# Optimization experiments

Hardware: AMD Instinct MI355X
Metric: run time of the kernel (lower is better)

## Reference

```python
import jax, jax.numpy as jnp
import numpy as np

REG = 1.0
LAM1 = REG * 0.1
LAM2 = REG * 0.15
TAU = 0.01
RHO = 1.99
SIGMA = 1.0 / TAU / 72.0


def epsilon(I):
    # I: (c,h,w,2) -> G: (c,h,w,4); symmetrized gradient stencil
    I0, I1 = I[..., 0], I[..., 1]
    g0 = I0 - jnp.pad(I0[:, :-1, :], ((0, 0), (1, 0), (0, 0)))
    g1 = jnp.pad(I0[:, :, 1:] - I0[:, :, :-1], ((0, 0), (0, 0), (1, 0)))
    g2 = I1 - jnp.pad(I1[:, :, :-1], ((0, 0), (0, 0), (1, 0)))
    g3 = jnp.pad(I1[:, 1:, :] - I1[:, :-1, :], ((0, 0), (0, 1), (0, 0)))
    return jnp.stack([g0, g1, g2, g3], axis=-1)


def epsilonT(G):
    # G: (c,h,w,4) -> I: (c,h,w,2); adjoint of epsilon
    g0, g1, g2, g3 = G[..., 0], G[..., 1], G[..., 2], G[..., 3]
    i0 = g0 - jnp.pad(g0[:, 1:, :], ((0, 0), (0, 1), (0, 0)))
    A = g1[:, :, 1:]
    i0 = i0 + jnp.pad(A, ((0, 0), (0, 0), (1, 0))) - jnp.pad(A, ((0, 0), (0, 0), (0, 1)))
    i1 = g2 - jnp.pad(g2[:, :, 1:], ((0, 0), (0, 0), (0, 1)))
    B = g3[:, :-1, :]
    i1 = i1 + jnp.pad(B, ((0, 0), (1, 0), (0, 0))) - jnp.pad(B, ((0, 0), (0, 1), (0, 0)))
    return jnp.stack([i0, i1], axis=-1)


def nabla(I):
    # I: (c,h,w) -> G: (c,h,w,2); forward differences, zero at far boundary
    g0 = jnp.pad(I[:, 1:, :] - I[:, :-1, :], ((0, 0), (0, 1), (0, 0)))
    g1 = jnp.pad(I[:, :, 1:] - I[:, :, :-1], ((0, 0), (0, 0), (0, 1)))
    return jnp.stack([g0, g1], axis=-1)


def nablaT(G):
    # G: (c,h,w,2) -> I: (c,h,w); negative divergence (adjoint of nabla)
    A = G[:, :-1, :, 0]
    B = G[:, :, :-1, 1]
    return (jnp.pad(A, ((0, 0), (1, 0), (0, 0))) - jnp.pad(A, ((0, 0), (0, 1), (0, 0)))
            + jnp.pad(B, ((0, 0), (0, 0), (1, 0))) - jnp.pad(B, ((0, 0), (0, 0), (0, 1))))


def prox_tau_fx(x, y):
    return (x + TAU * y) / (1.0 + TAU)


def prox_tau_fr(r):
    left = jnp.sqrt(jnp.sum(r ** 2, axis=3)) / (TAU * LAM1)
    return r - r / jnp.maximum(left, 1.0)[..., None]


def prox_sigma_g_conj(u):
    return u / jnp.maximum(jnp.sqrt(jnp.sum(u ** 2, axis=3)) / LAM2, 1.0)[..., None]


def setup_inputs() -> dict:
    key = jax.random.key(0)
    y = jax.random.normal(key, (3, 512, 512), dtype=jnp.float32)
    return {"y": y, "n_it_max": 30}


def reference(y, n_it_max):
    c, h, w = y.shape
    x2 = y
    r2 = jnp.zeros((c, h, w, 2), dtype=y.dtype)
    u2 = jnp.zeros((c, h, w, 4), dtype=y.dtype)

    def step(carry, _):
        x2, r2, u2 = carry
        tmp = TAU * epsilonT(u2)
        x = prox_tau_fx(x2 - nablaT(tmp), y)
        r = prox_tau_fr(r2 + tmp)
        u = prox_sigma_g_conj(u2 + SIGMA * epsilon(nabla(2.0 * x - x2) - (2.0 * r - r2)))
        x2 = x2 + RHO * (x - x2)
        r2 = r2 + RHO * (r - r2)
        u2 = u2 + RHO * (u - u2)
        return (x2, r2, u2), None

    (x2, r2, u2), _ = jax.lax.scan(step, (x2, r2, u2), None, length=n_it_max)
    return (x2, r2, u2)
```

## Files before the change

### kernel.cpp

```cpp
#include <hip/hip_runtime.h>
#include <type_traits>


#define H 512
#define W 512
#define C 3
#define HW (H * W)
#define CHW (C * H * W)
#define NPAIR 15

#define TW 64
#define TH 16

#define TAU     0.01f
#define LAM2    0.15f
#define RHO     1.99f
#define SIGMA   1.3888888888888888f
#define TL1     0.001f
#define INV_1PT (1.0f / 1.01f)

#define AR 22
#define AC 78
#define BR 18
#define BC 72
#define UR 20
#define UC 75

typedef _Float16 f16;
typedef __attribute__((ext_vector_type(4))) _Float16 h4;
typedef __attribute__((ext_vector_type(8))) _Float16 h8;


template <int MODE>
__global__ __launch_bounds__(256)
void fused2(const float* __restrict__ y,
            const float* __restrict__ srcX,
            const f16*   __restrict__ srcH,
            float*       __restrict__ dstX,
            f16*         __restrict__ dstH,
            float*       __restrict__ outp)
{
    __shared__ float sbA[3][AR][AC];
    __shared__ float sbB[3][BR][BC];
    __shared__ f16   su[UR][UC][4];

    const int tid = threadIdx.x;
    const int c   = blockIdx.z;
    const int i0  = blockIdx.y * TH;
    const int j0  = blockIdx.x * TW;
    const int cb  = c * HW;

    const bool edge = (MODE == 0) ||
                      (blockIdx.x == 0) || (blockIdx.x == W / TW - 1) ||
                      (blockIdx.y == 0) || (blockIdx.y == H / TH - 1);

    const f16* rSrc = srcH;
    const f16* uSrc = srcH + 2 * CHW;
    f16* rDst = dstH;
    f16* uDst = dstH ? dstH + 2 * CHW : nullptr;

    auto prox1 = [&](auto SAFE_c, int gi, int gjb,
                     const float* yv, const float* x2c, const float* r0c, const float* r1c,
                     const float* t0c, const float* t1c, const float* t0n, const float* t1w,
                     float* xb, float* rb0, float* rb1,
                     float* xn, float* rn0, float* rn1) {
        constexpr bool SAFE = decltype(SAFE_c)::value;
        const bool imH = SAFE ? true : (gi < H - 1);
        #pragma unroll
        for (int e = 0; e < 4; ++e) {
            const int gj = gjb + e;
            const bool jmW = SAFE ? true : (gj < W - 1);
            const float nT  = t0n[e] - (imH ? t0c[e] : 0.f) + t1w[e] - (jmW ? t1c[e] : 0.f);
            const float xv  = (x2c[e] - nT + TAU * yv[e]) * INV_1PT;
            xb[e] = 2.f * xv - x2c[e];
            const float rp0 = r0c[e] + t0c[e];
            const float rp1 = r1c[e] + t1c[e];
            const float ss  = rp0 * rp0 + rp1 * rp1;
            const float f   = 1.f - fminf(TL1 * rsqrtf(ss), 1.f);
            const float rv0 = rp0 * f, rv1 = rp1 * f;
            rb0[e] = 2.f * rv0 - r0c[e];
            rb1[e] = 2.f * rv1 - r1c[e];
            xn[e]  = x2c[e] + RHO * (xv - x2c[e]);
            rn0[e] = r0c[e] + RHO * (rv0 - r0c[e]);
            rn1[e] = r1c[e] + RHO * (rv1 - r1c[e]);
        }
    };

    auto tGlob = [&](auto SAFE_c, int gi, int gjb, int p,
                     float* t0c, float* t1c, float* t0n, float* t1w) {
        constexpr bool SAFE = decltype(SAFE_c)::value;
        const bool rowC  = SAFE || ((unsigned)gi < H);
        const bool cMain = SAFE || ((unsigned)gjb < W);
        const bool okC   = rowC && cMain;
        const bool rowN = SAFE || ((unsigned)(gi - 1) < H);
        const bool rowS = SAFE || ((unsigned)(gi + 1) < H);
        const bool cm1  = SAFE || ((unsigned)(gjb - 1) < W);
        const bool c4   = SAFE || ((unsigned)(gjb + 4) < W);
        const int pN = p - W, pS = p + W;
        auto L4 = [&](int pp, bool ok) -> h4 { h4 z = {}; if (ok) z = *(const h4*)(uSrc + 4 * pp); return z; };
        auto L8 = [&](int pp, bool ok) -> h8 { h8 z = {}; if (ok) z = *(const h8*)(uSrc + 4 * pp); return z; };
        const h4 nA = L4(pN - 1, rowN && cm1);
        const h8 nB = L8(pN,     rowN && cMain);
        const h8 nC = L8(pN + 2, rowN && cMain);
        const h4 nD = L4(pN + 4, rowN && c4);
        const h4 cA = L4(p - 1,  rowC && cm1);
        const h8 cB = L8(p,      okC);
        const h8 cC = L8(p + 2,  okC);
        const h4 cD = L4(p + 4,  rowC && c4);
        const h8 sB = L8(pS,     rowS && cMain);
        const h8 sC = L8(pS + 2, rowS && cMain);

        const float u0c[4] = {(float)cB[0], (float)cB[4], (float)cC[0], (float)cC[4]};
        const float u1c[5] = {(float)cB[1], (float)cB[5], (float)cC[1], (float)cC[5], (float)cD[1]};
        const float u2r[6] = {(float)cA[2], (float)cB[2], (float)cB[6], (float)cC[2], (float)cC[6], (float)cD[2]};
        const float u3c[5] = {(float)cA[3], (float)cB[3], (float)cB[7], (float)cC[3], (float)cC[7]};
        const float u0n[4] = {(float)nB[0], (float)nB[4], (float)nC[0], (float)nC[4]};
        const float u1n[5] = {(float)nB[1], (float)nB[5], (float)nC[1], (float)nC[5], (float)nD[1]};
        const float u3n[5] = {(float)nA[3], (float)nB[3], (float)nB[7], (float)nC[3], (float)nC[7]};
        const float u0s[4] = {(float)sB[0], (float)sB[4], (float)sC[0], (float)sC[4]};

        if constexpr (SAFE) {
            #pragma unroll
            for (int e = 0; e < 4; ++e) {
                t0c[e] = TAU * (u0c[e] - u0s[e] + u1c[e] - u1c[e + 1]);
                t1c[e] = TAU * (u2r[e + 1] - u2r[e + 2] + u3n[e + 1] - u3c[e + 1]);
                t0n[e] = TAU * (u0n[e] - u0c[e] + u1n[e] - u1n[e + 1]);
                t1w[e] = TAU * (u2r[e] - u2r[e + 1] + u3n[e] - u3c[e]);
            }
        } else {
            const bool im0 = gi > 0, imHl = gi < H - 1;
            #pragma unroll
            for (int e = 0; e < 4; ++e) {
                const int gj = gjb + e;
                const bool jm0 = gj > 0;
                t0c[e] = TAU * (u0c[e] - u0s[e] + (jm0 ? u1c[e] : 0.f) - u1c[e + 1]);
                t1c[e] = TAU * (u2r[e + 1] - u2r[e + 2] + u3n[e + 1] - (imHl ? u3c[e + 1] : 0.f));
                t0n[e] = im0 ? TAU * (u0n[e] - u0c[e] + (jm0 ? u1n[e] : 0.f) - u1n[e + 1]) : 0.f;
                t1w[e] = jm0 ? TAU * (u2r[e] - u2r[e + 1] + u3n[e] - (imHl ? u3c[e] : 0.f)) : 0.f;
            }
        }
    };

    auto loadA = [&](int rr, int s,
                     float* xA, float* xS, float* xN,
                     float* r0C, float* r0N, float* r1C, float* r1S) {
        const int lr = rr + 3, lc = s + 8;
        float4 v;
        xA[0] = sbA[0][lr][lc - 1];
        v = *(const float4*)&sbA[0][lr][lc]; xA[1]=v.x; xA[2]=v.y; xA[3]=v.z; xA[4]=v.w;
        xA[5] = sbA[0][lr][lc + 4];
        xS[0] = sbA[0][lr + 1][lc - 1];
        v = *(const float4*)&sbA[0][lr + 1][lc]; xS[1]=v.x; xS[2]=v.y; xS[3]=v.z; xS[4]=v.w;
        xS[5] = sbA[0][lr + 1][lc + 4];
        v = *(const float4*)&sbA[0][lr - 1][lc]; xN[0]=v.x; xN[1]=v.y; xN[2]=v.z; xN[3]=v.w;
        r0C[0] = sbA[1][lr][lc - 1];
        v = *(const float4*)&sbA[1][lr][lc]; r0C[1]=v.x; r0C[2]=v.y; r0C[3]=v.z; r0C[4]=v.w;
        v = *(const float4*)&sbA[1][lr - 1][lc]; r0N[0]=v.x; r0N[1]=v.y; r0N[2]=v.z; r0N[3]=v.w;
        r1C[0] = sbA[2][lr][lc - 1];
        v = *(const float4*)&sbA[2][lr][lc]; r1C[1]=v.x; r1C[2]=v.y; r1C[3]=v.z; r1C[4]=v.w;
        v = *(const float4*)&sbA[2][lr + 1][lc]; r1S[0]=v.x; r1S[1]=v.y; r1S[2]=v.z; r1S[3]=v.w;
    };

    auto s2core = [&](auto SAFE_c, int gi, int gjb,
                      const float* xA, const float* xS, const float* xN,
                      const float* r0C, const float* r0N, const float* r1C, const float* r1S,
                      const float* cu0, const float* cu1, const float* cu2, const float* cu3,
                      float* un0, float* un1, float* un2, float* un3) {
        constexpr bool SAFE = decltype(SAFE_c)::value;
        const bool im0 = SAFE ? true : (gi > 0);
        const bool imH = SAFE ? true : (gi < H - 1);
        #pragma unroll
        for (int e = 0; e < 4; ++e) {
            const int gj = gjb + e;
            const bool jm0 = SAFE ? true : (gj > 0);
            const bool jmW = SAFE ? true : (gj < W - 1);
            const float xC = xA[e + 1], xE = xA[e + 2], xW_ = xA[e];
            const float I0c = (imH ? xS[e + 1] - xC : 0.f) - r0C[e + 1];
            const float I0n = im0 ? (xC - xN[e] - r0N[e]) : 0.f;
            const float I0w = jm0 ? ((imH ? xS[e] - xW_ : 0.f) - r0C[e]) : 0.f;
            const float I1c = (jmW ? xE - xC : 0.f) - r1C[e + 1];
            const float I1w = jm0 ? (xC - xW_ - r1C[e]) : 0.f;
            const float I1s = imH ? ((jmW ? xS[e + 2] - xS[e + 1] : 0.f) - r1S[e]) : 0.f;
            const float g0 = I0c - I0n;
            const float g1 = jm0 ? (I0c - I0w) : 0.f;
            const float g2 = I1c - I1w;
            const float g3 = imH ? (I1s - I1c) : 0.f;
            const float up0 = cu0[e] + SIGMA * g0;
            const float up1 = cu1[e] + SIGMA * g1;
            const float up2 = cu2[e] + SIGMA * g2;
            const float up3 = cu3[e] + SIGMA * g3;
            const float ss  = up0 * up0 + up1 * up1 + up2 * up2 + up3 * up3;
            const float inv = fminf(LAM2 * rsqrtf(ss), 1.f);
            un0[e] = cu0[e] + RHO * (up0 * inv - cu0[e]);
            un1[e] = cu1[e] + RHO * (up1 * inv - cu1[e]);
            un2[e] = cu2[e] + RHO * (up2 * inv - cu2[e]);
            un3[e] = cu3[e] + RHO * (up3 * inv - cu3[e]);
        }
    };

    auto phaseA = [&](auto SAFE_c) {
        constexpr bool SAFE = decltype(SAFE_c)::value;
        for (int idx = tid; idx < AR * 18; idx += 256) {
            const int rw = idx / 18, rr = rw - 3;
            const int s  = 4 * (idx - rw * 18) - 4;
            const int gi = i0 + rr, gjb = j0 + s;
            const int p  = cb + gi * W + gjb;
            const bool rowC  = SAFE || ((unsigned)gi < H);
            const bool cMain = SAFE || ((unsigned)gjb < W);
            const bool okC   = rowC && cMain;

            float yv[4], x2c[4], r0c[4], r1c[4];
            if (okC) { *(float4*)yv = *(const float4*)(y + p); }
            else     { yv[0] = yv[1] = yv[2] = yv[3] = 0.f; }

            float t0c[4], t1c[4], t0n[4], t1w[4];
            if (MODE == 0) {
                #pragma unroll
                for (int e = 0; e < 4; ++e) {
                    x2c[e] = yv[e]; r0c[e] = 0.f; r1c[e] = 0.f;
                    t0c[e] = t1c[e] = t0n[e] = t1w[e] = 0.f;
                }
            } else {
                if (okC) {
                    *(float4*)x2c = *(const float4*)(srcX + p);
                    const h8 rv = *(const h8*)(rSrc + 2 * p);
                    #pragma unroll
                    for (int e = 0; e < 4; ++e) {
                        r0c[e] = (float)rv[2 * e];
                        r1c[e] = (float)rv[2 * e + 1];
                    }
                } else {
                    #pragma unroll
                    for (int e = 0; e < 4; ++e) { x2c[e] = 0.f; r0c[e] = 0.f; r1c[e] = 0.f; }
                }
                tGlob(SAFE_c, gi, gjb, p, t0c, t1c, t0n, t1w);
            }

            float xb[4], rb0[4], rb1[4], xn[4], rn0[4], rn1[4];
            prox1(SAFE_c, gi, gjb, yv, x2c, r0c, r1c, t0c, t1c, t0n, t1w,
                  xb, rb0, rb1, xn, rn0, rn1);

            *(float4*)&sbA[0][rr + 3][s + 8] = *(float4*)xb;
            *(float4*)&sbA[1][rr + 3][s + 8] = *(float4*)rb0;
            *(float4*)&sbA[2][rr + 3][s + 8] = *(float4*)rb1;
            if (rr >= -1 && rr <= 16) {
                *(float4*)&sbB[0][rr + 1][s + 4] = *(float4*)xn;
                *(float4*)&sbB[1][rr + 1][s + 4] = *(float4*)rn0;
                *(float4*)&sbB[2][rr + 1][s + 4] = *(float4*)rn1;
            }
        }
    };

    auto phaseB = [&](auto SAFE_c) {
        constexpr bool SAFE = decltype(SAFE_c)::value;
        for (int idx = tid; idx < UR * 18; idx += 256) {
            const int rw = idx / 18, rr = rw - 2;
            const int s  = 4 * (idx - rw * 18) - 4;
            const int gi = i0 + rr, gjb = j0 + s;
            const int p  = cb + gi * W + gjb;

            float xA[6], xS[6], xN[4], r0C[5], r0N[4], r1C[5], r1S[4];
            loadA(rr, s, xA, xS, xN, r0C, r0N, r1C, r1S);

            float cu0[4], cu1[4], cu2[4], cu3[4];
            if (MODE == 0) {
                #pragma unroll
                for (int e = 0; e < 4; ++e) { cu0[e] = cu1[e] = cu2[e] = cu3[e] = 0.f; }
            } else {
                const bool okC = SAFE || (((unsigned)gi < H) && ((unsigned)gjb < W));
                if (okC) {
                    const h8 a = *(const h8*)(uSrc + 4 * p);
                    const h8 b = *(const h8*)(uSrc + 4 * p + 8);
                    cu0[0]=(float)a[0]; cu1[0]=(float)a[1]; cu2[0]=(float)a[2]; cu3[0]=(float)a[3];
                    cu0[1]=(float)a[4]; cu1[1]=(float)a[5]; cu2[1]=(float)a[6]; cu3[1]=(float)a[7];
                    cu0[2]=(float)b[0]; cu1[2]=(float)b[1]; cu2[2]=(float)b[2]; cu3[2]=(float)b[3];
                    cu0[3]=(float)b[4]; cu1[3]=(float)b[5]; cu2[3]=(float)b[6]; cu3[3]=(float)b[7];
                } else {
                    #pragma unroll
                    for (int e = 0; e < 4; ++e) { cu0[e] = cu1[e] = cu2[e] = cu3[e] = 0.f; }
                }
            }

            float un0[4], un1[4], un2[4], un3[4];
            s2core(SAFE_c, gi, gjb, xA, xS, xN, r0C, r0N, r1C, r1S,
                   cu0, cu1, cu2, cu3, un0, un1, un2, un3);

            const int ur = rr + 2, uc = s + 6;
            if constexpr (SAFE) {
                h8 w0, w1;
                #pragma unroll
                for (int e = 0; e < 2; ++e) {
                    w0[4*e+0]=(f16)un0[e]; w0[4*e+1]=(f16)un1[e];
                    w0[4*e+2]=(f16)un2[e]; w0[4*e+3]=(f16)un3[e];
                }
                #pragma unroll
                for (int e = 2; e < 4; ++e) {
                    w1[4*(e-2)+0]=(f16)un0[e]; w1[4*(e-2)+1]=(f16)un1[e];
                    w1[4*(e-2)+2]=(f16)un2[e]; w1[4*(e-2)+3]=(f16)un3[e];
                }
                *(h8*)&su[ur][uc][0]     = w0;
                *(h8*)&su[ur][uc + 2][0] = w1;
            } else {
                #pragma unroll
                for (int e = 0; e < 4; ++e) {
                    const int gj = gjb + e;
                    const bool ok = ((unsigned)gi < H) && ((unsigned)gj < W);
                    h4 hv = {};
                    if (ok) { hv[0]=(f16)un0[e]; hv[1]=(f16)un1[e]; hv[2]=(f16)un2[e]; hv[3]=(f16)un3[e]; }
                    *(h4*)&su[ur][uc + e][0] = hv;
                }
            }
        }
    };

    auto phaseC = [&](auto SAFE_c) {
        constexpr bool SAFE = decltype(SAFE_c)::value;
        for (int idx = tid; idx < BR * 18; idx += 256) {
            const int rw = idx / 18, rr = rw - 1;
            const int s  = 4 * (idx - rw * 18) - 4;
            const int gi = i0 + rr, gjb = j0 + s;
            const int p  = cb + gi * W + gjb;
            const bool okC = SAFE || (((unsigned)gi < H) && ((unsigned)gjb < W));

            float yv[4];
            if (okC) { *(float4*)yv = *(const float4*)(y + p); }
            else     { yv[0] = yv[1] = yv[2] = yv[3] = 0.f; }

            float x2c[4], r0c[4], r1c[4];
            *(float4*)x2c = *(const float4*)&sbB[0][rr + 1][s + 4];
            *(float4*)r0c = *(const float4*)&sbB[1][rr + 1][s + 4];
            *(float4*)r1c = *(const float4*)&sbB[2][rr + 1][s + 4];

            h4 pN_[6], pC_[6], pS_[4];
            #pragma unroll
            for (int k = 0; k < 6; ++k) {
                pN_[k] = *(const h4*)&su[rr + 1][s + 5 + k][0];
                pC_[k] = *(const h4*)&su[rr + 2][s + 5 + k][0];
            }
            #pragma unroll
            for (int k = 0; k < 4; ++k)
                pS_[k] = *(const h4*)&su[rr + 3][s + 6 + k][0];

            const float u0c[4] = {(float)pC_[1][0], (float)pC_[2][0], (float)pC_[3][0], (float)pC_[4][0]};
            const float u1c[5] = {(float)pC_[1][1], (float)pC_[2][1], (float)pC_[3][1], (float)pC_[4][1], (float)pC_[5][1]};
            const float u2r[6] = {(float)pC_[0][2], (float)pC_[1][2], (float)pC_[2][2], (float)pC_[3][2], (float)pC_[4][2], (float)pC_[5][2]};
            const float u3c[5] = {(float)pC_[0][3], (float)pC_[1][3], (float)pC_[2][3], (float)pC_[3][3], (float)pC_[4][3]};
            const float u0n[4] = {(float)pN_[1][0], (float)pN_[2][0], (float)pN_[3][0], (float)pN_[4][0]};
            const float u1n[5] = {(float)pN_[1][1], (float)pN_[2][1], (float)pN_[3][1], (float)pN_[4][1], (float)pN_[5][1]};
            const float u3n[5] = {(float)pN_[0][3], (float)pN_[1][3], (float)pN_[2][3], (float)pN_[3][3], (float)pN_[4][3]};
            const float u0s[4] = {(float)pS_[0][0], (float)pS_[1][0], (float)pS_[2][0], (float)pS_[3][0]};

            float t0c[4], t1c[4], t0n[4], t1w[4];
            if constexpr (SAFE) {
                #pragma unroll
                for (int e = 0; e < 4; ++e) {
                    t0c[e] = TAU * (u0c[e] - u0s[e] + u1c[e] - u1c[e + 1]);
                    t1c[e] = TAU * (u2r[e + 1] - u2r[e + 2] + u3n[e + 1] - u3c[e + 1]);
                    t0n[e] = TAU * (u0n[e] - u0c[e] + u1n[e] - u1n[e + 1]);
                    t1w[e] = TAU * (u2r[e] - u2r[e + 1] + u3n[e] - u3c[e]);
                }
            } else {
                const bool im0 = gi > 0, imHl = gi < H - 1;
                #pragma unroll
                for (int e = 0; e < 4; ++e) {
                    const int gj = gjb + e;
                    const bool jm0 = gj > 0;
                    t0c[e] = TAU * (u0c[e] - u0s[e] + (jm0 ? u1c[e] : 0.f) - u1c[e + 1]);
                    t1c[e] = TAU * (u2r[e + 1] - u2r[e + 2] + u3n[e + 1] - (imHl ? u3c[e + 1] : 0.f));
                    t0n[e] = im0 ? TAU * (u0n[e] - u0c[e] + (jm0 ? u1n[e] : 0.f) - u1n[e + 1]) : 0.f;
                    t1w[e] = jm0 ? TAU * (u2r[e] - u2r[e + 1] + u3n[e] - (imHl ? u3c[e] : 0.f)) : 0.f;
                }
            }

            float xb[4], rb0[4], rb1[4], xn[4], rn0[4], rn1[4];
            prox1(SAFE_c, gi, gjb, yv, x2c, r0c, r1c, t0c, t1c, t0n, t1w,
                  xb, rb0, rb1, xn, rn0, rn1);

            *(float4*)&sbA[0][rr + 3][s + 8] = *(float4*)xb;
            *(float4*)&sbA[1][rr + 3][s + 8] = *(float4*)rb0;
            *(float4*)&sbA[2][rr + 3][s + 8] = *(float4*)rb1;

            if ((unsigned)rr < 16 && (unsigned)s < 64) {
                if (MODE == 2) {
                    *(float4*)(outp + p) = *(float4*)xn;
                    *(float4*)(outp + CHW + 2 * p)     = make_float4(rn0[0], rn1[0], rn0[1], rn1[1]);
                    *(float4*)(outp + CHW + 2 * p + 4) = make_float4(rn0[2], rn1[2], rn0[3], rn1[3]);
                } else {
                    *(float4*)(dstX + p) = *(float4*)xn;
                    h8 hr;
                    #pragma unroll
                    for (int e = 0; e < 4; ++e) {
                        hr[2 * e]     = (f16)rn0[e];
                        hr[2 * e + 1] = (f16)rn1[e];
                    }
                    *(h8*)(rDst + 2 * p) = hr;
                }
            }
        }
    };

    if (!edge) phaseA(std::true_type{});  else phaseA(std::false_type{});
    __syncthreads();
    if (!edge) phaseB(std::true_type{});  else phaseB(std::false_type{});
    __syncthreads();
    if (!edge) phaseC(std::true_type{});  else phaseC(std::false_type{});
    __syncthreads();

    {
        const int rr = tid >> 4;
        const int s  = 4 * (tid & 15);
        const int gi = i0 + rr, gjb = j0 + s;
        const int p  = cb + gi * W + gjb;

        float xA[6], xS[6], xN[4], r0C[5], r0N[4], r1C[5], r1S[4];
        loadA(rr, s, xA, xS, xN, r0C, r0N, r1C, r1S);

        float cu0[4], cu1[4], cu2[4], cu3[4];
        {
            const h8 a = *(const h8*)&su[rr + 2][s + 6][0];
            const h8 b = *(const h8*)&su[rr + 2][s + 8][0];
            cu0[0]=(float)a[0]; cu1[0]=(float)a[1]; cu2[0]=(float)a[2]; cu3[0]=(float)a[3];
            cu0[1]=(float)a[4]; cu1[1]=(float)a[5]; cu2[1]=(float)a[6]; cu3[1]=(float)a[7];
            cu0[2]=(float)b[0]; cu1[2]=(float)b[1]; cu2[2]=(float)b[2]; cu3[2]=(float)b[3];
            cu0[3]=(float)b[4]; cu1[3]=(float)b[5]; cu2[3]=(float)b[6]; cu3[3]=(float)b[7];
        }

        float un0[4], un1[4], un2[4], un3[4];
        if (!edge)
            s2core(std::true_type{},  gi, gjb, xA, xS, xN, r0C, r0N, r1C, r1S,
                   cu0, cu1, cu2, cu3, un0, un1, un2, un3);
        else
            s2core(std::false_type{}, gi, gjb, xA, xS, xN, r0C, r0N, r1C, r1S,
                   cu0, cu1, cu2, cu3, un0, un1, un2, un3);

        if (MODE == 2) {
            #pragma unroll
            for (int e = 0; e < 4; ++e)
                *(float4*)(outp + 3 * CHW + 4 * (p + e)) =
                    make_float4(un0[e], un1[e], un2[e], un3[e]);
        } else {
            h8 w0, w1;
            #pragma unroll
            for (int e = 0; e < 2; ++e) {
                w0[4*e+0]=(f16)un0[e]; w0[4*e+1]=(f16)un1[e];
                w0[4*e+2]=(f16)un2[e]; w0[4*e+3]=(f16)un3[e];
            }
            #pragma unroll
            for (int e = 2; e < 4; ++e) {
                w1[4*(e-2)+0]=(f16)un0[e]; w1[4*(e-2)+1]=(f16)un1[e];
                w1[4*(e-2)+2]=(f16)un2[e]; w1[4*(e-2)+3]=(f16)un3[e];
            }
            *(h8*)(uDst + 4 * p)     = w0;
            *(h8*)(uDst + 4 * p + 8) = w1;
        }
    }
}

extern "C" void kernel_launch(void* const* d_in, const int* in_sizes, int n_in,
                              void* d_out, int out_size, void* d_ws, size_t ws_size,
                              hipStream_t stream) {
    const float* y = (const float*)d_in[0];
    float* out = (float*)d_out;

    float* x0 = (float*)d_ws;
    float* x1 = x0 + CHW;
    f16*   h0 = (f16*)(x1 + CHW);
    f16*   h1 = h0 + 6 * CHW;

    dim3 blk(256, 1, 1);
    dim3 grd(W / TW, H / TH, C);

    fused2<0><<<grd, blk, 0, stream>>>(y, nullptr, nullptr, x0, h0, nullptr);
    for (int i = 1; i < NPAIR - 1; ++i) {
        const bool even = (i % 2 == 0);
        float* sx = even ? x1 : x0;  f16* sh = even ? h1 : h0;
        float* dx = even ? x0 : x1;  f16* dh = even ? h0 : h1;
        fused2<1><<<grd, blk, 0, stream>>>(y, sx, sh, dx, dh, nullptr);
    }
    fused2<2><<<grd, blk, 0, stream>>>(y, x1, h1, nullptr, nullptr, out);
}
```

Measured before the change: 299.7 us.

## Stage u halo tile in LDS once and read stencil from shared memory

Before the fused stages run, each block cooperatively loads the u dual-variable halo tile (with zero padding at image edges) from global memory into a larger shared buffer. The per-thread scattered global h4/h8 loads in phase A and phase B are replaced by shared-memory reads, and phase C's register reads now share the same helper. This removes redundant overlapping global reads of u across threads. In exchange it adds a barrier, grows the LDS footprint (UR 24, UC 76), and phase B now overwrites the u tile in place.

```diff
diff --git a/kernel.cpp b/kernel.cpp
--- a/kernel.cpp
+++ b/kernel.cpp
@@ -23,8 +23,8 @@
 #define AC 78
 #define BR 18
 #define BC 72
-#define UR 20
-#define UC 75
+#define UR 24
+#define UC 76
 
 typedef _Float16 f16;
 typedef __attribute__((ext_vector_type(4))) _Float16 h4;
@@ -58,6 +58,40 @@
     const f16* uSrc = srcH + 2 * CHW;
     f16* rDst = dstH;
     f16* uDst = dstH ? dstH + 2 * CHW : nullptr;
+
+    if (MODE != 0) {
+        if (!edge) {
+            for (int t = tid; t < UR * 38; t += 256) {
+                const int ur = t / 38;
+                const int k  = t - ur * 38;
+                const int gi = i0 + ur - 4;
+                const int gc = j0 - 6 + 2 * k;
+                *(h8*)&su[ur][2 * k][0] =
+                    *(const h8*)(uSrc + 4 * (cb + gi * W + gc));
+            }
+        } else {
+            for (int t = tid; t < UR * 38; t += 256) {
+                const int ur = t / 38;
+                const int k  = t - ur * 38;
+                const int gi = i0 + ur - 4;
+                const int gc = j0 - 6 + 2 * k;
+                const bool rok = (unsigned)gi < H;
+                const bool ok0 = rok && ((unsigned)gc < W);
+                const bool ok1 = rok && ((unsigned)(gc + 1) < W);
+                if (ok0 && ok1) {
+                    *(h8*)&su[ur][2 * k][0] =
+                        *(const h8*)(uSrc + 4 * (cb + gi * W + gc));
+                } else {
+                    h4 a = {}, b = {};
+                    if (ok0) a = *(const h4*)(uSrc + 4 * (cb + gi * W + gc));
+                    if (ok1) b = *(const h4*)(uSrc + 4 * (cb + gi * W + gc + 1));
+                    *(h4*)&su[ur][2 * k][0]     = a;
+                    *(h4*)&su[ur][2 * k + 1][0] = b;
+                }
+            }
+        }
+        __syncthreads();
+    }
 
     auto prox1 = [&](auto SAFE_c, int gi, int gjb,
                      const float* yv, const float* x2c, const float* r0c, const float* r1c,
@@ -86,46 +120,40 @@
         }
     };
 
-    auto tGlob = [&](auto SAFE_c, int gi, int gjb, int p,
-                     float* t0c, float* t1c, float* t0n, float* t1w) {
-        constexpr bool SAFE = decltype(SAFE_c)::value;
-        const bool rowC  = SAFE || ((unsigned)gi < H);
-        const bool cMain = SAFE || ((unsigned)gjb < W);
-        const bool okC   = rowC && cMain;
-        const bool rowN = SAFE || ((unsigned)(gi - 1) < H);
-        const bool rowS = SAFE || ((unsigned)(gi + 1) < H);
-        const bool cm1  = SAFE || ((unsigned)(gjb - 1) < W);
-        const bool c4   = SAFE || ((unsigned)(gjb + 4) < W);
-        const int pN = p - W, pS = p + W;
-        auto L4 = [&](int pp, bool ok) -> h4 { h4 z = {}; if (ok) z = *(const h4*)(uSrc + 4 * pp); return z; };
-        auto L8 = [&](int pp, bool ok) -> h8 { h8 z = {}; if (ok) z = *(const h8*)(uSrc + 4 * pp); return z; };
-        const h4 nA = L4(pN - 1, rowN && cm1);
-        const h8 nB = L8(pN,     rowN && cMain);
-        const h8 nC = L8(pN + 2, rowN && cMain);
-        const h4 nD = L4(pN + 4, rowN && c4);
-        const h4 cA = L4(p - 1,  rowC && cm1);
-        const h8 cB = L8(p,      okC);
-        const h8 cC = L8(p + 2,  okC);
-        const h4 cD = L4(p + 4,  rowC && c4);
-        const h8 sB = L8(pS,     rowS && cMain);
-        const h8 sC = L8(pS + 2, rowS && cMain);
-
-        const float u0c[4] = {(float)cB[0], (float)cB[4], (float)cC[0], (float)cC[4]};
-        const float u1c[5] = {(float)cB[1], (float)cB[5], (float)cC[1], (float)cC[5], (float)cD[1]};
-        const float u2r[6] = {(float)cA[2], (float)cB[2], (float)cB[6], (float)cC[2], (float)cC[6], (float)cD[2]};
-        const float u3c[5] = {(float)cA[3], (float)cB[3], (float)cB[7], (float)cC[3], (float)cC[7]};
-        const float u0n[4] = {(float)nB[0], (float)nB[4], (float)nC[0], (float)nC[4]};
-        const float u1n[5] = {(float)nB[1], (float)nB[5], (float)nC[1], (float)nC[5], (float)nD[1]};
-        const float u3n[5] = {(float)nA[3], (float)nB[3], (float)nB[7], (float)nC[3], (float)nC[7]};
-        const float u0s[4] = {(float)sB[0], (float)sB[4], (float)sC[0], (float)sC[4]};
-
+    auto uRow6 = [&](int ur, int s, float* u0, float* u1, float* u2, float* u3) {
+        const h8 q0 = *(const h8*)&su[ur][s + 4][0];
+        const h8 q1 = *(const h8*)&su[ur][s + 6][0];
+        const h8 q2 = *(const h8*)&su[ur][s + 8][0];
+        const h8 q3 = *(const h8*)&su[ur][s + 10][0];
+        u0[0]=(float)q0[4]; u1[0]=(float)q0[5]; u2[0]=(float)q0[6]; u3[0]=(float)q0[7];
+        u0[1]=(float)q1[0]; u1[1]=(float)q1[1]; u2[1]=(float)q1[2]; u3[1]=(float)q1[3];
+        u0[2]=(float)q1[4]; u1[2]=(float)q1[5]; u2[2]=(float)q1[6]; u3[2]=(float)q1[7];
+        u0[3]=(float)q2[0]; u1[3]=(float)q2[1]; u2[3]=(float)q2[2]; u3[3]=(float)q2[3];
+        u0[4]=(float)q2[4]; u1[4]=(float)q2[5]; u2[4]=(float)q2[6]; u3[4]=(float)q2[7];
+        u0[5]=(float)q3[0]; u1[5]=(float)q3[1]; u2[5]=(float)q3[2]; u3[5]=(float)q3[3];
+    };
+    auto uRow4u0 = [&](int ur, int s, float* u0) {
+        const h8 q1 = *(const h8*)&su[ur][s + 6][0];
+        const h8 q2 = *(const h8*)&su[ur][s + 8][0];
+        u0[0]=(float)q1[0]; u0[1]=(float)q1[4]; u0[2]=(float)q2[0]; u0[3]=(float)q2[4];
+    };
+
+    auto tLds = [&](auto SAFE_c, int rr, int s, int gi, int gjb,
+                    float* t0c, float* t1c, float* t0n, float* t1w) {
+        constexpr bool SAFE = decltype(SAFE_c)::value;
+        float N0[6], N1[6], N2[6], N3[6];
+        float C0[6], C1[6], C2[6], C3[6];
+        float S0[4];
+        uRow6(rr + 3, s, N0, N1, N2, N3);
+        uRow6(rr + 4, s, C0, C1, C2, C3);
+        uRow4u0(rr + 5, s, S0);
         if constexpr (SAFE) {
             #pragma unroll
             for (int e = 0; e < 4; ++e) {
-                t0c[e] = TAU * (u0c[e] - u0s[e] + u1c[e] - u1c[e + 1]);
-                t1c[e] = TAU * (u2r[e + 1] - u2r[e + 2] + u3n[e + 1] - u3c[e + 1]);
-                t0n[e] = TAU * (u0n[e] - u0c[e] + u1n[e] - u1n[e + 1]);
-                t1w[e] = TAU * (u2r[e] - u2r[e + 1] + u3n[e] - u3c[e]);
+                t0c[e] = TAU * (C0[e + 1] - S0[e] + C1[e + 1] - C1[e + 2]);
+                t1c[e] = TAU * (C2[e + 1] - C2[e + 2] + N3[e + 1] - C3[e + 1]);
+                t0n[e] = TAU * (N0[e + 1] - C0[e + 1] + N1[e + 1] - N1[e + 2]);
+                t1w[e] = TAU * (C2[e] - C2[e + 1] + N3[e] - C3[e]);
             }
         } else {
             const bool im0 = gi > 0, imHl = gi < H - 1;
@@ -133,10 +161,10 @@
             for (int e = 0; e < 4; ++e) {
                 const int gj = gjb + e;
                 const bool jm0 = gj > 0;
-                t0c[e] = TAU * (u0c[e] - u0s[e] + (jm0 ? u1c[e] : 0.f) - u1c[e + 1]);
-                t1c[e] = TAU * (u2r[e + 1] - u2r[e + 2] + u3n[e + 1] - (imHl ? u3c[e + 1] : 0.f));
-                t0n[e] = im0 ? TAU * (u0n[e] - u0c[e] + (jm0 ? u1n[e] : 0.f) - u1n[e + 1]) : 0.f;
-                t1w[e] = jm0 ? TAU * (u2r[e] - u2r[e + 1] + u3n[e] - (imHl ? u3c[e] : 0.f)) : 0.f;
+                t0c[e] = TAU * (C0[e + 1] - S0[e] + (jm0 ? C1[e + 1] : 0.f) - C1[e + 2]);
+                t1c[e] = TAU * (C2[e + 1] - C2[e + 2] + N3[e + 1] - (imHl ? C3[e + 1] : 0.f));
+                t0n[e] = im0 ? TAU * (N0[e + 1] - C0[e + 1] + (jm0 ? N1[e + 1] : 0.f) - N1[e + 2]) : 0.f;
+                t1w[e] = jm0 ? TAU * (C2[e] - C2[e + 1] + N3[e] - (imHl ? C3[e] : 0.f)) : 0.f;
             }
         }
     };
@@ -198,6 +226,15 @@
         }
     };
 
+    auto cuRead = [&](int rr, int s, float* cu0, float* cu1, float* cu2, float* cu3) {
+        const h8 a = *(const h8*)&su[rr + 4][s + 6][0];
+        const h8 b = *(const h8*)&su[rr + 4][s + 8][0];
+        cu0[0]=(float)a[0]; cu1[0]=(float)a[1]; cu2[0]=(float)a[2]; cu3[0]=(float)a[3];
+        cu0[1]=(float)a[4]; cu1[1]=(float)a[5]; cu2[1]=(float)a[6]; cu3[1]=(float)a[7];
+        cu0[2]=(float)b[0]; cu1[2]=(float)b[1]; cu2[2]=(float)b[2]; cu3[2]=(float)b[3];
+        cu0[3]=(float)b[4]; cu1[3]=(float)b[5]; cu2[3]=(float)b[6]; cu3[3]=(float)b[7];
+    };
+
     auto phaseA = [&](auto SAFE_c) {
         constexpr bool SAFE = decltype(SAFE_c)::value;
         for (int idx = tid; idx < AR * 18; idx += 256) {
@@ -233,7 +270,7 @@
                     #pragma unroll
                     for (int e = 0; e < 4; ++e) { x2c[e] = 0.f; r0c[e] = 0.f; r1c[e] = 0.f; }
                 }
-                tGlob(SAFE_c, gi, gjb, p, t0c, t1c, t0n, t1w);
+                tLds(SAFE_c, rr, s, gi, gjb, t0c, t1c, t0n, t1w);
             }
 
             float xb[4], rb0[4], rb1[4], xn[4], rn0[4], rn1[4];
@@ -253,11 +290,10 @@
 
     auto phaseB = [&](auto SAFE_c) {
         constexpr bool SAFE = decltype(SAFE_c)::value;
-        for (int idx = tid; idx < UR * 18; idx += 256) {
+        for (int idx = tid; idx < 20 * 18; idx += 256) {
             const int rw = idx / 18, rr = rw - 2;
             const int s  = 4 * (idx - rw * 18) - 4;
             const int gi = i0 + rr, gjb = j0 + s;
-            const int p  = cb + gi * W + gjb;
 
             float xA[6], xS[6], xN[4], r0C[5], r0N[4], r1C[5], r1S[4];
             loadA(rr, s, xA, xS, xN, r0C, r0N, r1C, r1S);
@@ -267,25 +303,14 @@
                 #pragma unroll
                 for (int e = 0; e < 4; ++e) { cu0[e] = cu1[e] = cu2[e] = cu3[e] = 0.f; }
             } else {
-                const bool okC = SAFE || (((unsigned)gi < H) && ((unsigned)gjb < W));
-                if (okC) {
-                    const h8 a = *(const h8*)(uSrc + 4 * p);
-                    const h8 b = *(const h8*)(uSrc + 4 * p + 8);
-                    cu0[0]=(float)a[0]; cu1[0]=(float)a[1]; cu2[0]=(float)a[2]; cu3[0]=(float)a[3];
-                    cu0[1]=(float)a[4]; cu1[1]=(float)a[5]; cu2[1]=(float)a[6]; cu3[1]=(float)a[7];
-                    cu0[2]=(float)b[0]; cu1[2]=(float)b[1]; cu2[2]=(float)b[2]; cu3[2]=(float)b[3];
-                    cu0[3]=(float)b[4]; cu1[3]=(float)b[5]; cu2[3]=(float)b[6]; cu3[3]=(float)b[7];
-                } else {
-                    #pragma unroll
-                    for (int e = 0; e < 4; ++e) { cu0[e] = cu1[e] = cu2[e] = cu3[e] = 0.f; }
-                }
+                cuRead(rr, s, cu0, cu1, cu2, cu3);
             }
 
             float un0[4], un1[4], un2[4], un3[4];
             s2core(SAFE_c, gi, gjb, xA, xS, xN, r0C, r0N, r1C, r1S,
                    cu0, cu1, cu2, cu3, un0, un1, un2, un3);
 
-            const int ur = rr + 2, uc = s + 6;
+            const int ur = rr + 4, uc = s + 6;
             if constexpr (SAFE) {
                 h8 w0, w1;
                 #pragma unroll
@@ -331,46 +356,8 @@
             *(float4*)r0c = *(const float4*)&sbB[1][rr + 1][s + 4];
             *(float4*)r1c = *(const float4*)&sbB[2][rr + 1][s + 4];
 
-            h4 pN_[6], pC_[6], pS_[4];
-            #pragma unroll
-            for (int k = 0; k < 6; ++k) {
-                pN_[k] = *(const h4*)&su[rr + 1][s + 5 + k][0];
-                pC_[k] = *(const h4*)&su[rr + 2][s + 5 + k][0];
-            }
-            #pragma unroll
-            for (int k = 0; k < 4; ++k)
-                pS_[k] = *(const h4*)&su[rr + 3][s + 6 + k][0];
-
-            const float u0c[4] = {(float)pC_[1][0], (float)pC_[2][0], (float)pC_[3][0], (float)pC_[4][0]};
-            const float u1c[5] = {(float)pC_[1][1], (float)pC_[2][1], (float)pC_[3][1], (float)pC_[4][1], (float)pC_[5][1]};
-            const float u2r[6] = {(float)pC_[0][2], (float)pC_[1][2], (float)pC_[2][2], (float)pC_[3][2], (float)pC_[4][2], (float)pC_[5][2]};
-            const float u3c[5] = {(float)pC_[0][3], (float)pC_[1][3], (float)pC_[2][3], (float)pC_[3][3], (float)pC_[4][3]};
-            const float u0n[4] = {(float)pN_[1][0], (float)pN_[2][0], (float)pN_[3][0], (float)pN_[4][0]};
-            const float u1n[5] = {(float)pN_[1][1], (float)pN_[2][1], (float)pN_[3][1], (float)pN_[4][1], (float)pN_[5][1]};
-            const float u3n[5] = {(float)pN_[0][3], (float)pN_[1][3], (float)pN_[2][3], (float)pN_[3][3], (float)pN_[4][3]};
-            const float u0s[4] = {(float)pS_[0][0], (float)pS_[1][0], (float)pS_[2][0], (float)pS_[3][0]};
-
             float t0c[4], t1c[4], t0n[4], t1w[4];
-            if constexpr (SAFE) {
-                #pragma unroll
-                for (int e = 0; e < 4; ++e) {
-                    t0c[e] = TAU * (u0c[e] - u0s[e] + u1c[e] - u1c[e + 1]);
-                    t1c[e] = TAU * (u2r[e + 1] - u2r[e + 2] + u3n[e + 1] - u3c[e + 1]);
-                    t0n[e] = TAU * (u0n[e] - u0c[e] + u1n[e] - u1n[e + 1]);
-                    t1w[e] = TAU * (u2r[e] - u2r[e + 1] + u3n[e] - u3c[e]);
-                }
-            } else {
-                const bool im0 = gi > 0, imHl = gi < H - 1;
-                #pragma unroll
-                for (int e = 0; e < 4; ++e) {
-                    const int gj = gjb + e;
-                    const bool jm0 = gj > 0;
-                    t0c[e] = TAU * (u0c[e] - u0s[e] + (jm0 ? u1c[e] : 0.f) - u1c[e + 1]);
-                    t1c[e] = TAU * (u2r[e + 1] - u2r[e + 2] + u3n[e + 1] - (imHl ? u3c[e + 1] : 0.f));
-                    t0n[e] = im0 ? TAU * (u0n[e] - u0c[e] + (jm0 ? u1n[e] : 0.f) - u1n[e + 1]) : 0.f;
-                    t1w[e] = jm0 ? TAU * (u2r[e] - u2r[e + 1] + u3n[e] - (imHl ? u3c[e] : 0.f)) : 0.f;
-                }
-            }
+            tLds(SAFE_c, rr, s, gi, gjb, t0c, t1c, t0n, t1w);
 
             float xb[4], rb0[4], rb1[4], xn[4], rn0[4], rn1[4];
             prox1(SAFE_c, gi, gjb, yv, x2c, r0c, r1c, t0c, t1c, t0n, t1w,
@@ -416,14 +403,7 @@
         loadA(rr, s, xA, xS, xN, r0C, r0N, r1C, r1S);
 
         float cu0[4], cu1[4], cu2[4], cu3[4];
-        {
-            const h8 a = *(const h8*)&su[rr + 2][s + 6][0];
-            const h8 b = *(const h8*)&su[rr + 2][s + 8][0];
-            cu0[0]=(float)a[0]; cu1[0]=(float)a[1]; cu2[0]=(float)a[2]; cu3[0]=(float)a[3];
-            cu0[1]=(float)a[4]; cu1[1]=(float)a[5]; cu2[1]=(float)a[6]; cu3[1]=(float)a[7];
-            cu0[2]=(float)b[0]; cu1[2]=(float)b[1]; cu2[2]=(float)b[2]; cu3[2]=(float)b[3];
-            cu0[3]=(float)b[4]; cu1[3]=(float)b[5]; cu2[3]=(float)b[6]; cu3[3]=(float)b[7];
-        }
+        cuRead(rr, s, cu0, cu1, cu2, cu3);
 
         float un0[4], un1[4], un2[4], un3[4];
         if (!edge)
```

Measured after the change: 309.9 us. +3.4%, slower.
